# Kernel optimization log

Hardware: AMD Instinct MI355X
Metric: run time of the kernel (lower is better)

The kernel has to match this reference:

```python
import jax, jax.numpy as jnp
import numpy as np
from jax import lax

WINDOW = 9
N_INT = 1000
WMSE_WEIGHTS = np.array([1.0, 2.0, 5.0, 10.0, 30.0], dtype=np.float32)
WMSE_THRESH = np.array([0.5, 2.0, 5.0, 10.0], dtype=np.float32)
LOSS_W = np.array([1e-4, 1.0], dtype=np.float32)


def setup_inputs() -> dict:
    key = jax.random.key(0)
    k1, k2 = jax.random.split(key)
    shape = (4, 1, 128, 128)
    return {
        "prediction": jax.random.normal(k1, shape, dtype=jnp.float32),
        "target": jax.random.normal(k2, shape, dtype=jnp.float32),
    }


def _box_mean(x, win):
    # Equivalent to the original shift-and-accumulate running mean: box sum over
    # in-bounds neighbors (edge-corrected mean). x: [B, 1, H, W].
    pad = win // 2
    k = jnp.ones((1, 1, win, win), x.dtype)
    num = lax.conv_general_dilated(x, k, (1, 1), [(pad, pad), (pad, pad)])
    ones = jnp.ones((1, 1) + x.shape[-2:], x.dtype)
    den = lax.conv_general_dilated(ones, k, (1, 1), [(pad, pad), (pad, pad)])
    return num / den


def _wmse(pred, tgt):
    # Threshold-weighted MSE: weight chosen by the largest threshold <= target.
    w = jnp.full_like(tgt, WMSE_WEIGHTS[0])
    for i in range(len(WMSE_THRESH)):
        w = jnp.where(tgt >= WMSE_THRESH[i], WMSE_WEIGHTS[i + 1], w)
    return jnp.mean(w * (pred - tgt) ** 2)


def _crps(pred, tgt, n):
    # Deterministic CRPS via numeric integration over n points spanning the
    # global data range: integral (H(x - pred) - H(x - tgt))^2 dx per pixel.
    lo = jnp.minimum(pred.min(), tgt.min())
    hi = jnp.maximum(pred.max(), tgt.max())
    x = jnp.linspace(lo, hi, n)
    dx = (hi - lo) / (n - 1)
    p = pred.reshape(-1)
    t = tgt.reshape(-1)
    Fp = x[:, None] >= p[None, :]  # [N_INT, n_pixels]
    Ft = x[:, None] >= t[None, :]
    sq = (Fp ^ Ft).astype(pred.dtype)  # (Fp - Ft)^2 for 0/1 indicators
    return jnp.mean(sq.sum(axis=0) * dx)


def reference(prediction, target):
    pred_dist = prediction - _box_mean(prediction, WINDOW)
    tgt_dist = target - _box_mean(target, WINDOW)
    wmse = _wmse(prediction, target)
    crps = _crps(pred_dist, tgt_dist, N_INT)
    return LOSS_W[0] * wmse + LOSS_W[1] * crps
```

## Files before the change

### kernel.cpp

```cpp
#include <hip/hip_runtime.h>

#define SCOPE_AGENT __HIP_MEMORY_SCOPE_AGENT


__global__ __launch_bounds__(256) void SPL_one(const float* __restrict__ pred,
                                               const float* __restrict__ tgt,
                                               float* __restrict__ ws,
                                               float* __restrict__ out) {
    __shared__ float sP[1280], sT[1280];
    __shared__ float vsP[256], vsT[256];
    __shared__ float red[12];
    __shared__ int   redi[4];
    __shared__ float bcast[2];

    float*    psum   = ws;
    float*    pmn    = ws + 256;
    float*    pmx    = ws + 512;
    int*      pcnt   = (int*)(ws + 768);
    unsigned* flags1 = (unsigned*)(ws + 1024);
    unsigned* flags2 = (unsigned*)(ws + 1280);
    const unsigned MAGIC1 = 0xA11C0DE5u;
    const unsigned MAGIC2 = 0x5EC0DE22u;

    int b = blockIdx.x;
    int t = threadIdx.x;
    int m  = b >> 6;
    int r2 = (b & 63) << 1;
    const float* p = pred + (m << 14);
    const float* q = tgt  + (m << 14);

#pragma unroll
    for (int s = 0; s < 5; ++s) {
        int k   = t + s * 256;
        int rr  = k >> 7;
        int cc  = k & 127;
        int grw = r2 - 4 + rr;
        bool ok = (unsigned)grw < 128u;
        sP[k] = ok ? p[(grw << 7) + cc] : 0.f;
        sT[k] = ok ? q[(grw << 7) + cc] : 0.f;
    }
    __syncthreads();

    int orow = t >> 7;
    int col  = t & 127;
    int row  = r2 + orow;

    float vp = 0.f, vt = 0.f;
    int vb = orow * 128 + col;
#pragma unroll
    for (int di = 0; di < 9; ++di) {
        vp += sP[vb + di * 128];
        vt += sT[vb + di * 128];
    }
    vsP[t] = vp; vsT[t] = vt;
    __syncthreads();

    float sp = 0.f, st = 0.f;
    int rbase = t & ~127;
#pragma unroll
    for (int dj = -4; dj <= 4; ++dj) {
        int jj = col + dj;
        if ((unsigned)jj < 128u) { sp += vsP[rbase + jj]; st += vsT[rbase + jj]; }
    }

    int   rc  = min(row, 4) + min(127 - row, 4) + 1;
    int   cn  = min(col, 4) + min(127 - col, 4) + 1;
    float den = (float)(rc * cn);
    float pv  = sP[(orow + 4) * 128 + col];
    float tv  = sT[(orow + 4) * 128 + col];
    float pd  = pv - sp / den;
    float td  = tv - st / den;

    float w = 1.f;
    if (tv >= 0.5f) w = 2.f;
    if (tv >= 2.f)  w = 5.f;
    if (tv >= 5.f)  w = 10.f;
    if (tv >= 10.f) w = 30.f;
    float d  = pv - tv;
    float s  = w * d * d;
    float mn = fminf(pd, td);
    float mx = fmaxf(pd, td);

    for (int o = 32; o > 0; o >>= 1) {
        s  += __shfl_down(s, o, 64);
        mn  = fminf(mn, __shfl_down(mn, o, 64));
        mx  = fmaxf(mx, __shfl_down(mx, o, 64));
    }
    int lane = t & 63, wid = t >> 6;
    if (lane == 0) { red[wid] = s; red[4 + wid] = mn; red[8 + wid] = mx; }
    __syncthreads();
    if (t == 0) {
        float bs  = red[0] + red[1] + red[2] + red[3];
        float bmn = fminf(fminf(red[4], red[5]), fminf(red[6], red[7]));
        float bmx = fmaxf(fmaxf(red[8], red[9]), fmaxf(red[10], red[11]));
        __hip_atomic_store(&psum[b], bs,  __ATOMIC_RELAXED, SCOPE_AGENT);
        __hip_atomic_store(&pmn[b],  bmn, __ATOMIC_RELAXED, SCOPE_AGENT);
        __hip_atomic_store(&pmx[b],  bmx, __ATOMIC_RELAXED, SCOPE_AGENT);
        __hip_atomic_store(&flags1[b], MAGIC1, __ATOMIC_RELEASE, SCOPE_AGENT);
    }

    if (t < 64) {
        for (int i = t; i < 256; i += 64) {
            while (__hip_atomic_load(&flags1[i], __ATOMIC_ACQUIRE, SCOPE_AGENT) != MAGIC1)
                __builtin_amdgcn_s_sleep(1);
        }
    }
    __syncthreads();

    float mn2 = __hip_atomic_load(&pmn[t], __ATOMIC_RELAXED, SCOPE_AGENT);
    float mx2 = __hip_atomic_load(&pmx[t], __ATOMIC_RELAXED, SCOPE_AGENT);
    for (int o = 32; o > 0; o >>= 1) {
        mn2 = fminf(mn2, __shfl_down(mn2, o, 64));
        mx2 = fmaxf(mx2, __shfl_down(mx2, o, 64));
    }
    if (lane == 0) { red[4 + wid] = mn2; red[8 + wid] = mx2; }
    __syncthreads();
    if (t == 0) {
        bcast[0] = fminf(fminf(red[4], red[5]), fminf(red[6], red[7]));
        bcast[1] = fmaxf(fmaxf(red[8], red[9]), fmaxf(red[10], red[11]));
    }
    __syncthreads();
    float lo = bcast[0], hi = bcast[1];
    float dx = (hi - lo) / 999.0f;
    float inv_dx = 1.0f / dx;

    float a0 = fminf(pd, td);
    float b0 = fmaxf(pd, td);
    int ka = (int)ceilf((a0 - lo) * inv_dx);
    int kb = (int)ceilf((b0 - lo) * inv_dx);
    ka = max(ka, 0); kb = min(kb, 1000);
    int cnt = max(kb - ka, 0);

    for (int o = 32; o > 0; o >>= 1) cnt += __shfl_down(cnt, o, 64);
    if (lane == 0) redi[wid] = cnt;
    __syncthreads();
    if (t == 0) {
        int bc = redi[0] + redi[1] + redi[2] + redi[3];
        __hip_atomic_store(&pcnt[b], bc, __ATOMIC_RELAXED, SCOPE_AGENT);
        __hip_atomic_store(&flags2[b], MAGIC2, __ATOMIC_RELEASE, SCOPE_AGENT);
    }

    if (b == 0) {
        if (t < 64) {
            for (int i = t; i < 256; i += 64) {
                while (__hip_atomic_load(&flags2[i], __ATOMIC_ACQUIRE, SCOPE_AGENT) != MAGIC2)
                    __builtin_amdgcn_s_sleep(1);
            }
        }
        __syncthreads();

        int   c  = __hip_atomic_load(&pcnt[t], __ATOMIC_RELAXED, SCOPE_AGENT);
        float ss = __hip_atomic_load(&psum[t], __ATOMIC_RELAXED, SCOPE_AGENT);
        for (int o = 32; o > 0; o >>= 1) {
            c  += __shfl_down(c, o, 64);
            ss += __shfl_down(ss, o, 64);
        }
        if (lane == 0) { redi[wid] = c; red[wid] = ss; }
        __syncthreads();
        if (t == 0) {
            long long tot = (long long)redi[0] + redi[1] + redi[2] + redi[3];
            float  wmse = (red[0] + red[1] + red[2] + red[3]) * (1.0f / 65536.0f);
            double crps = (double)tot * (double)dx / 65536.0;
            out[0] = 1e-4f * wmse + (float)crps;
        }
    }
}

extern "C" void kernel_launch(void* const* d_in, const int* in_sizes, int n_in,
                              void* d_out, int out_size, void* d_ws, size_t ws_size,
                              hipStream_t stream) {
    const float* pred = (const float*)d_in[0];
    const float* tgt  = (const float*)d_in[1];
    float* ws  = (float*)d_ws;
    float* out = (float*)d_out;

    SPL_one<<<256, 256, 0, stream>>>(pred, tgt, ws, out);
}
```

Baseline: 75.26 us.

## Replace all-to-all grid barrier with single detector block broadcasting global min/max

```diff
diff --git a/kernel.cpp b/kernel.cpp
--- a/kernel.cpp
+++ b/kernel.cpp
@@ -19,8 +19,12 @@
     int*      pcnt   = (int*)(ws + 768);
     unsigned* flags1 = (unsigned*)(ws + 1024);
     unsigned* flags2 = (unsigned*)(ws + 1280);
+    unsigned* goarr  = (unsigned*)(ws + 1536);
+    float*    lohi   = ws + 1792;
     const unsigned MAGIC1 = 0xA11C0DE5u;
     const unsigned MAGIC2 = 0x5EC0DE22u;
+    const unsigned MAGICG = 0x60F1A600u;
+    const int DETECTOR = 255;
 
     int b = blockIdx.x;
     int t = threadIdx.x;
@@ -93,37 +97,51 @@
         float bs  = red[0] + red[1] + red[2] + red[3];
         float bmn = fminf(fminf(red[4], red[5]), fminf(red[6], red[7]));
         float bmx = fmaxf(fmaxf(red[8], red[9]), fmaxf(red[10], red[11]));
-        __hip_atomic_store(&psum[b], bs,  __ATOMIC_RELAXED, SCOPE_AGENT);
-        __hip_atomic_store(&pmn[b],  bmn, __ATOMIC_RELAXED, SCOPE_AGENT);
-        __hip_atomic_store(&pmx[b],  bmx, __ATOMIC_RELAXED, SCOPE_AGENT);
+        psum[b] = bs;
+        pmn[b]  = bmn;
+        pmx[b]  = bmx;
         __hip_atomic_store(&flags1[b], MAGIC1, __ATOMIC_RELEASE, SCOPE_AGENT);
     }
 
-    if (t < 64) {
-        for (int i = t; i < 256; i += 64) {
-            while (__hip_atomic_load(&flags1[i], __ATOMIC_ACQUIRE, SCOPE_AGENT) != MAGIC1)
+    float lo, hi;
+    if (b == DETECTOR) {
+        while (__hip_atomic_load(&flags1[t], __ATOMIC_RELAXED, SCOPE_AGENT) != MAGIC1)
+            __builtin_amdgcn_s_sleep(1);
+        __syncthreads();
+        __builtin_amdgcn_fence(__ATOMIC_ACQUIRE, "agent");
+        float mn2 = pmn[t], mx2 = pmx[t];
+        for (int o = 32; o > 0; o >>= 1) {
+            mn2 = fminf(mn2, __shfl_down(mn2, o, 64));
+            mx2 = fmaxf(mx2, __shfl_down(mx2, o, 64));
+        }
+        if (lane == 0) { red[4 + wid] = mn2; red[8 + wid] = mx2; }
+        __syncthreads();
+        if (t == 0) {
+            float l = fminf(fminf(red[4], red[5]), fminf(red[6], red[7]));
+            float h = fmaxf(fmaxf(red[8], red[9]), fmaxf(red[10], red[11]));
+            lohi[0] = l; lohi[1] = h;
+            bcast[0] = l; bcast[1] = h;
+        }
+        __syncthreads();
+        if (t < 8) {
+            __builtin_amdgcn_fence(__ATOMIC_RELEASE, "agent");
+            __hip_atomic_store(&goarr[t * 32], MAGICG, __ATOMIC_RELAXED, SCOPE_AGENT);
+        }
+        lo = bcast[0]; hi = bcast[1];
+    } else {
+        if (t == 0) {
+            while (__hip_atomic_load(&goarr[(b & 7) * 32], __ATOMIC_RELAXED, SCOPE_AGENT) != MAGICG)
                 __builtin_amdgcn_s_sleep(1);
         }
+        __syncthreads();
+        __builtin_amdgcn_fence(__ATOMIC_ACQUIRE, "agent");
+        if (t == 0) { bcast[0] = lohi[0]; bcast[1] = lohi[1]; }
+        __syncthreads();
+        lo = bcast[0]; hi = bcast[1];
     }
-    __syncthreads();
 
-    float mn2 = __hip_atomic_load(&pmn[t], __ATOMIC_RELAXED, SCOPE_AGENT);
-    float mx2 = __hip_atomic_load(&pmx[t], __ATOMIC_RELAXED, SCOPE_AGENT);
-    for (int o = 32; o > 0; o >>= 1) {
-        mn2 = fminf(mn2, __shfl_down(mn2, o, 64));
-        mx2 = fmaxf(mx2, __shfl_down(mx2, o, 64));
-    }
-    if (lane == 0) { red[4 + wid] = mn2; red[8 + wid] = mx2; }
-    __syncthreads();
-    if (t == 0) {
-        bcast[0] = fminf(fminf(red[4], red[5]), fminf(red[6], red[7]));
-        bcast[1] = fmaxf(fmaxf(red[8], red[9]), fmaxf(red[10], red[11]));
-    }
-    __syncthreads();
-    float lo = bcast[0], hi = bcast[1];
     float dx = (hi - lo) / 999.0f;
     float inv_dx = 1.0f / dx;
-
     float a0 = fminf(pd, td);
     float b0 = fmaxf(pd, td);
     int ka = (int)ceilf((a0 - lo) * inv_dx);
@@ -135,22 +153,17 @@
     if (lane == 0) redi[wid] = cnt;
     __syncthreads();
     if (t == 0) {
-        int bc = redi[0] + redi[1] + redi[2] + redi[3];
-        __hip_atomic_store(&pcnt[b], bc, __ATOMIC_RELAXED, SCOPE_AGENT);
+        pcnt[b] = redi[0] + redi[1] + redi[2] + redi[3];
         __hip_atomic_store(&flags2[b], MAGIC2, __ATOMIC_RELEASE, SCOPE_AGENT);
     }
 
     if (b == 0) {
-        if (t < 64) {
-            for (int i = t; i < 256; i += 64) {
-                while (__hip_atomic_load(&flags2[i], __ATOMIC_ACQUIRE, SCOPE_AGENT) != MAGIC2)
-                    __builtin_amdgcn_s_sleep(1);
-            }
-        }
+        while (__hip_atomic_load(&flags2[t], __ATOMIC_RELAXED, SCOPE_AGENT) != MAGIC2)
+            __builtin_amdgcn_s_sleep(1);
         __syncthreads();
-
-        int   c  = __hip_atomic_load(&pcnt[t], __ATOMIC_RELAXED, SCOPE_AGENT);
-        float ss = __hip_atomic_load(&psum[t], __ATOMIC_RELAXED, SCOPE_AGENT);
+        __builtin_amdgcn_fence(__ATOMIC_ACQUIRE, "agent");
+        int   c  = pcnt[t];
+        float ss = psum[t];
         for (int o = 32; o > 0; o >>= 1) {
             c  += __shfl_down(c, o, 64);
             ss += __shfl_down(ss, o, 64);
```

New measurement: 74.57 us. No clear change (-0.9%).
